# Kernel tuning notes

Hardware: AMD Instinct MI355X
Metric: run time of the kernel (lower is better)

The kernel has to match this reference:

```python
import jax, jax.numpy as jnp
import numpy as np

B, T, C = 2, 4096, 512
H = 8
D = C // H  # head_dim = 64


def setup_inputs() -> dict:
    key = jax.random.key(0)
    ks = jax.random.split(key, 9)
    s = 0.02
    return {
        "x": jax.random.normal(ks[0], (B, T, C), dtype=jnp.float32),
        "wq": jax.random.normal(ks[1], (C, C), dtype=jnp.float32) * s,
        "bq": jnp.zeros((C,), dtype=jnp.float32),
        "wk": jax.random.normal(ks[2], (C, C), dtype=jnp.float32) * s,
        "bk": jnp.zeros((C,), dtype=jnp.float32),
        "wv": jax.random.normal(ks[3], (C, C), dtype=jnp.float32) * s,
        "bv": jnp.zeros((C,), dtype=jnp.float32),
        "wo": jax.random.normal(ks[4], (C, C), dtype=jnp.float32) * s,
        "bo": jnp.zeros((C,), dtype=jnp.float32),
    }


def reference(x, wq, bq, wk, bk, wv, bv, wo, bo):
    Bx, Tx, Cx = x.shape
    # projections: y = x @ W^T + b (torch Linear convention: W is [out, in])
    q = (x @ wq.T + bq).reshape(Bx, Tx, H, D).transpose(0, 2, 1, 3)  # [B,H,T,D]
    k = (x @ wk.T + bk).reshape(Bx, Tx, H, D).transpose(0, 2, 1, 3)
    v = (x @ wv.T + bv).reshape(Bx, Tx, H, D).transpose(0, 2, 1, 3)
    scores = jnp.einsum("bhqd,bhkd->bhqk", q, k) * (D ** -0.5)  # [B,H,T,T]
    causal = jnp.tril(jnp.ones((Tx, Tx), dtype=bool))
    scores = jnp.where(causal, scores, -jnp.inf)
    weights = jax.nn.softmax(scores, axis=-1)
    o = jnp.einsum("bhqk,bhkd->bhqd", weights, v)  # [B,H,T,D]
    o = o.transpose(0, 2, 1, 3).reshape(Bx, Tx, Cx)
    return o @ wo.T + bo
```

## Files before the change

kernel.cpp:

```cpp
#include <hip/hip_runtime.h>
#include <math.h>

static constexpr int Bb = 2;
static constexpr int Tt = 4096;
static constexpr int Cc = 512;
static constexpr int Hh = 8;
static constexpr int Dd = 64;
static constexpr int Mtot = Bb * Tt;

#define QSCALE 0.1803368801111f
#define NTICK 1024

typedef __attribute__((ext_vector_type(8)))  short   short8;
typedef __attribute__((ext_vector_type(4)))  float   f32x4;
typedef __attribute__((ext_vector_type(16))) float   f32x16;
typedef __attribute__((ext_vector_type(4)))  unsigned int   uint4v;
typedef __attribute__((ext_vector_type(4)))  unsigned short ushort4v;

__device__ inline unsigned short f2bf(float f) {
    unsigned int u = __float_as_uint(f);
    u += 0x7fffu + ((u >> 16) & 1u);
    return (unsigned short)(u >> 16);
}
__device__ inline float bf2f(unsigned short u) {
    return __uint_as_float((unsigned int)u << 16);
}

__device__ inline unsigned int cvtpk_bf16(float a, float b) {
    unsigned int r;
    asm("v_cvt_pk_bf16_f32 %0, %1, %2" : "=v"(r) : "v"(a), "v"(b));
    return r;
}

__device__ inline int SW(int row) { return (row ^ (row >> 3)) & 7; }

__device__ inline void gload16(const void* g, void* lds) {
    __builtin_amdgcn_global_load_lds(
        (const __attribute__((address_space(1))) void*)g,
        (__attribute__((address_space(3))) void*)lds, 16, 0, 0);
}

__global__ __launch_bounds__(256)
void cast_f32_bf16(const float* __restrict__ src, unsigned short* __restrict__ dst,
                   int* __restrict__ ctr) {
    if (blockIdx.x == 0 && threadIdx.x == 0) *ctr = 0;
    const size_t i = ((size_t)blockIdx.x * 256 + threadIdx.x) * 8;
    const float4 a = *reinterpret_cast<const float4*>(src + i);
    const float4 b = *reinterpret_cast<const float4*>(src + i + 4);
    short8 o;
    o[0] = (short)f2bf(a.x); o[1] = (short)f2bf(a.y);
    o[2] = (short)f2bf(a.z); o[3] = (short)f2bf(a.w);
    o[4] = (short)f2bf(b.x); o[5] = (short)f2bf(b.y);
    o[6] = (short)f2bf(b.z); o[7] = (short)f2bf(b.w);
    *reinterpret_cast<short8*>(dst + i) = o;
}

__global__ __launch_bounds__(256)
void cast_w4(const float* __restrict__ w0, const float* __restrict__ w1,
             const float* __restrict__ w2, const float* __restrict__ w3,
             unsigned short* __restrict__ dst) {
    const float* srcs[4] = {w0, w1, w2, w3};
    const float* s = srcs[blockIdx.y];
    unsigned short* d = dst + (size_t)blockIdx.y * (Cc * Cc);
    const size_t i = ((size_t)blockIdx.x * 256 + threadIdx.x) * 8;
    const float4 a = *reinterpret_cast<const float4*>(s + i);
    const float4 b = *reinterpret_cast<const float4*>(s + i + 4);
    short8 o;
    o[0] = (short)f2bf(a.x); o[1] = (short)f2bf(a.y);
    o[2] = (short)f2bf(a.z); o[3] = (short)f2bf(a.w);
    o[4] = (short)f2bf(b.x); o[5] = (short)f2bf(b.y);
    o[6] = (short)f2bf(b.z); o[7] = (short)f2bf(b.w);
    *reinterpret_cast<short8*>(d + i) = o;
}

__global__ __launch_bounds__(256)
void proj_qkv(const unsigned short* __restrict__ A, const unsigned short* __restrict__ Wall,
              const float* __restrict__ bq, const float* __restrict__ bk,
              const float* __restrict__ bv,
              unsigned short* __restrict__ qo, unsigned short* __restrict__ ko,
              unsigned short* __restrict__ vo) {
    __shared__ unsigned short As[128][32];
    __shared__ unsigned short Bs[128][32];

    const int which = blockIdx.z;
    const unsigned short* Wb = Wall + (size_t)which * Cc * Cc;
    const float* bias = (which == 0) ? bq : (which == 1) ? bk : bv;
    unsigned short* outp = (which == 0) ? qo : (which == 1) ? ko : vo;
    const float scale = (which == 0) ? QSCALE : 1.0f;

    const int tid = threadIdx.x;
    const int lane = tid & 63;
    const int w = tid >> 6;
    const int wr = w >> 1, wc = w & 1;
    const int l15 = lane & 15, lg = lane >> 4;
    const int m0 = blockIdx.x * 128, n0 = blockIdx.y * 128;

    f32x4 acc[4][4] = {};

    for (int k0 = 0; k0 < Cc; k0 += 32) {
        #pragma unroll
        for (int i = 0; i < 2; ++i) {
            const int idx = tid + i * 256;
            const int row = idx >> 2, g = idx & 3;
            *reinterpret_cast<short8*>(&As[row][g * 8]) =
                *reinterpret_cast<const short8*>(&A[(size_t)(m0 + row) * Cc + k0 + g * 8]);
            *reinterpret_cast<short8*>(&Bs[row][g * 8]) =
                *reinterpret_cast<const short8*>(&Wb[(size_t)(n0 + row) * Cc + k0 + g * 8]);
        }
        __syncthreads();
        short8 a[4], b[4];
        #pragma unroll
        for (int mi = 0; mi < 4; ++mi)
            a[mi] = *reinterpret_cast<const short8*>(&As[wr * 64 + mi * 16 + l15][lg * 8]);
        #pragma unroll
        for (int nj = 0; nj < 4; ++nj)
            b[nj] = *reinterpret_cast<const short8*>(&Bs[wc * 64 + nj * 16 + l15][lg * 8]);
        #pragma unroll
        for (int mi = 0; mi < 4; ++mi)
            #pragma unroll
            for (int nj = 0; nj < 4; ++nj)
                acc[mi][nj] = __builtin_amdgcn_mfma_f32_16x16x32_bf16(a[mi], b[nj], acc[mi][nj], 0, 0, 0);
        __syncthreads();
    }

    #pragma unroll
    for (int mi = 0; mi < 4; ++mi) {
        #pragma unroll
        for (int nj = 0; nj < 4; ++nj) {
            const int col = n0 + wc * 64 + nj * 16 + l15;
            const float bvv = bias[col];
            if (which == 2) {
                const int mbase = m0 + wr * 64 + mi * 16 + lg * 4;
                const int b_ = mbase >> 12, t = mbase & (Tt - 1);
                const int h = col >> 6, d = col & 63;
                ushort4v o;
                #pragma unroll
                for (int r = 0; r < 4; ++r)
                    o[r] = f2bf(acc[mi][nj][r] + bvv);
                *reinterpret_cast<ushort4v*>(
                    &outp[(((size_t)b_ * Hh + h) * Dd + d) * Tt + t]) = o;
            } else {
                #pragma unroll
                for (int r = 0; r < 4; ++r) {
                    const int row = m0 + wr * 64 + mi * 16 + lg * 4 + r;
                    const int b_ = row >> 12, t = row & (Tt - 1);
                    const int h = col >> 6, d = col & 63;
                    outp[(((size_t)b_ * Hh + h) * Tt + t) * Dd + d] =
                        f2bf((acc[mi][nj][r] + bvv) * scale);
                }
            }
        }
    }
}

__global__ __launch_bounds__(256)
void proj_out(const unsigned short* __restrict__ A, const unsigned short* __restrict__ Wb,
              const float* __restrict__ bias, float* __restrict__ outp) {
    __shared__ unsigned short As[128][32];
    __shared__ unsigned short Bs[128][32];

    const int tid = threadIdx.x;
    const int lane = tid & 63;
    const int w = tid >> 6;
    const int wr = w >> 1, wc = w & 1;
    const int l15 = lane & 15, lg = lane >> 4;
    const int m0 = blockIdx.x * 128, n0 = blockIdx.y * 128;

    f32x4 acc[4][4] = {};

    for (int k0 = 0; k0 < Cc; k0 += 32) {
        #pragma unroll
        for (int i = 0; i < 2; ++i) {
            const int idx = tid + i * 256;
            const int row = idx >> 2, g = idx & 3;
            *reinterpret_cast<short8*>(&As[row][g * 8]) =
                *reinterpret_cast<const short8*>(&A[(size_t)(m0 + row) * Cc + k0 + g * 8]);
            *reinterpret_cast<short8*>(&Bs[row][g * 8]) =
                *reinterpret_cast<const short8*>(&Wb[(size_t)(n0 + row) * Cc + k0 + g * 8]);
        }
        __syncthreads();
        short8 a[4], b[4];
        #pragma unroll
        for (int mi = 0; mi < 4; ++mi)
            a[mi] = *reinterpret_cast<const short8*>(&As[wr * 64 + mi * 16 + l15][lg * 8]);
        #pragma unroll
        for (int nj = 0; nj < 4; ++nj)
            b[nj] = *reinterpret_cast<const short8*>(&Bs[wc * 64 + nj * 16 + l15][lg * 8]);
        #pragma unroll
        for (int mi = 0; mi < 4; ++mi)
            #pragma unroll
            for (int nj = 0; nj < 4; ++nj)
                acc[mi][nj] = __builtin_amdgcn_mfma_f32_16x16x32_bf16(a[mi], b[nj], acc[mi][nj], 0, 0, 0);
        __syncthreads();
    }

    #pragma unroll
    for (int mi = 0; mi < 4; ++mi) {
        #pragma unroll
        for (int nj = 0; nj < 4; ++nj) {
            const int col = n0 + wc * 64 + nj * 16 + l15;
            const float bv = bias[col];
            #pragma unroll
            for (int r = 0; r < 4; ++r) {
                const int row = m0 + wr * 64 + mi * 16 + lg * 4 + r;
                outp[(size_t)row * Cc + col] = acc[mi][nj][r] + bv;
            }
        }
    }
}

__global__ __launch_bounds__(512)
void attn_mfma(const unsigned short* __restrict__ qb, const unsigned short* __restrict__ kb,
               const unsigned short* __restrict__ vtb,
               unsigned short* __restrict__ opart, float* __restrict__ lp,
               int* __restrict__ ctr) {
    __shared__ unsigned short Ks[3][64][64];
    __shared__ unsigned short Vts[3][64][64];
    __shared__ int tkt;

    const int tid = threadIdx.x;
    const int w = tid >> 6;
    const int lane = tid & 63;
    const int l31 = lane & 31, hi = lane >> 5;

    const int r0 = (w << 3) + (lane >> 3);
    const int gk0 = ((lane & 7) ^ SW(r0)) * 8;

    for (;;) {
        __syncthreads();
        if (tid == 0) tkt = atomicAdd(ctr, 1);
        __syncthreads();
        const int t = tkt;
        if (t >= NTICK) break;

        const int qt = 15 - (t >> 6);
        const int ch = (t >> 4) & 3;
        const int bh = t & 15;
        const int t0 = (qt + 1) * ch;
        const int t1 = (qt + 1) * (ch + 1);

        const int qg = qt * 256 + w * 32 + l31;

        short8 qf[4];
        {
            const unsigned short* qp = qb + ((size_t)bh * Tt + qg) * Dd + hi * 8;
            #pragma unroll
            for (int sl = 0; sl < 4; ++sl)
                qf[sl] = *reinterpret_cast<const short8*>(qp + sl * 16);
        }

        const unsigned short* kb_h = kb + (size_t)bh * Tt * Dd;
        const unsigned short* vt_h = vtb + (size_t)bh * Dd * Tt;

        auto STAGE = [&](int kt_, int slot) {
            const int n64 = kt_ * 64;
            gload16(kb_h + (size_t)(n64 + r0) * Dd + gk0, &Ks[slot][(w << 3)][0]);
            gload16(vt_h + (size_t)r0 * Tt + n64 + gk0, &Vts[slot][(w << 3)][0]);
        };

        f32x16 oacc[2] = {};
        float lrow = 0.f;

        const int qmax_w = qt * 256 + w * 32 + 31;
        const int qmin_w = qt * 256 + w * 32;

        STAGE(t0, 0);
        if (t0 + 1 < t1) STAGE(t0 + 1, 1);

        int cur = 0;
        for (int kt = t0; kt < t1; ++kt) {
            if (kt + 1 < t1) {
                asm volatile("s_waitcnt vmcnt(2)" ::: "memory");
            } else {
                asm volatile("s_waitcnt vmcnt(0)" ::: "memory");
            }
            __builtin_amdgcn_s_barrier();
            __builtin_amdgcn_sched_barrier(0);

            if (kt + 2 < t1) {
                const int stg = (cur + 2 >= 3) ? (cur - 1) : (cur + 2);
                STAGE(kt + 2, stg);
            }

            if (kt * 64 <= qmax_w) {
                f32x16 sacc[2];
                __builtin_amdgcn_s_setprio(1);
                #pragma unroll
                for (int f = 0; f < 2; ++f) {
                    f32x16 z = {};
                    const int krow = f * 32 + l31;
                    const int sw = SW(krow);
                    #pragma unroll
                    for (int sl = 0; sl < 4; ++sl) {
                        const short8 kf = *reinterpret_cast<const short8*>(
                            &Ks[cur][krow][((2 * sl + hi) ^ sw) * 8]);
                        z = __builtin_amdgcn_mfma_f32_32x32x16_bf16(kf, qf[sl], z, 0, 0, 0);
                    }
                    sacc[f] = z;
                }
                __builtin_amdgcn_s_setprio(0);

                if (kt * 64 + 63 > qmin_w) {
                    #pragma unroll
                    for (int f = 0; f < 2; ++f)
                        #pragma unroll
                        for (int r = 0; r < 16; ++r) {
                            const int kvg = kt * 64 + f * 32 + (r & 3) + 8 * (r >> 2) + 4 * hi;
                            if (kvg > qg) sacc[f][r] = -INFINITY;
                        }
                }

                #pragma unroll
                for (int f = 0; f < 2; ++f)
                    #pragma unroll
                    for (int r = 0; r < 16; ++r)
                        sacc[f][r] = exp2f(sacc[f][r]);

                float t16[16];
                #pragma unroll
                for (int r = 0; r < 16; ++r) t16[r] = sacc[0][r] + sacc[1][r];
                #pragma unroll
                for (int r = 0; r < 8; ++r) t16[r] += t16[r + 8];
                #pragma unroll
                for (int r = 0; r < 4; ++r) t16[r] += t16[r + 4];
                t16[0] += t16[2];
                t16[1] += t16[3];
                lrow += t16[0] + t16[1];

                #pragma unroll
                for (int f = 0; f < 2; ++f) {
                    #pragma unroll
                    for (int s2 = 0; s2 < 2; ++s2) {
                        const int b0 = s2 * 8;
                        unsigned int c01 = cvtpk_bf16(sacc[f][b0 + 0], sacc[f][b0 + 1]);
                        unsigned int c23 = cvtpk_bf16(sacc[f][b0 + 2], sacc[f][b0 + 3]);
                        unsigned int c45 = cvtpk_bf16(sacc[f][b0 + 4], sacc[f][b0 + 5]);
                        unsigned int c67 = cvtpk_bf16(sacc[f][b0 + 6], sacc[f][b0 + 7]);
                        asm("v_permlane32_swap_b32 %0, %1" : "+v"(c01), "+v"(c45));
                        asm("v_permlane32_swap_b32 %0, %1" : "+v"(c23), "+v"(c67));
                        uint4v paw;
                        paw[0] = c01; paw[1] = c23; paw[2] = c45; paw[3] = c67;
                        const short8 pa = *reinterpret_cast<short8*>(&paw);
                        const int g = 4 * f + 2 * s2;
                        __builtin_amdgcn_s_setprio(1);
                        #pragma unroll
                        for (int nb = 0; nb < 2; ++nb) {
                            const int vrow = nb * 32 + l31;
                            const short8 vf = *reinterpret_cast<const short8*>(
                                &Vts[cur][vrow][((g + hi) ^ SW(vrow)) * 8]);
                            oacc[nb] = __builtin_amdgcn_mfma_f32_32x32x16_bf16(pa, vf, oacc[nb], 0, 0, 0);
                        }
                        __builtin_amdgcn_s_setprio(0);
                    }
                }
            }

            cur = (cur == 2) ? 0 : cur + 1;
        }

        const float lf = lrow + __shfl_xor(lrow, 32);
        const size_t pbase = ((size_t)ch * 16 + bh) * Tt;
        if (hi == 0) lp[pbase + qg] = lf;
        #pragma unroll
        for (int r = 0; r < 16; ++r) {
            const int qr = (r & 3) + 8 * (r >> 2) + 4 * hi;
            const int tg = qt * 256 + w * 32 + qr;
            unsigned short* dst = opart + (pbase + tg) * 64 + l31;
            dst[0]  = f2bf(oacc[0][r]);
            dst[32] = f2bf(oacc[1][r]);
        }
    }
}

__global__ __launch_bounds__(256)
void combine(const unsigned short* __restrict__ opart, const float* __restrict__ lp,
             unsigned short* __restrict__ ob) {
    const int tid = threadIdx.x;
    const int row = (int)blockIdx.x * 16 + (tid >> 4);
    const int c4 = (tid & 15) * 4;
    const size_t cs = (size_t)16 * Tt;

    const float inv = 1.f / (lp[row] + lp[cs + row] + lp[2 * cs + row] + lp[3 * cs + row]);

    const ushort4v p0 = *reinterpret_cast<const ushort4v*>(&opart[(0 * cs + row) * 64 + c4]);
    const ushort4v p1 = *reinterpret_cast<const ushort4v*>(&opart[(1 * cs + row) * 64 + c4]);
    const ushort4v p2 = *reinterpret_cast<const ushort4v*>(&opart[(2 * cs + row) * 64 + c4]);
    const ushort4v p3 = *reinterpret_cast<const ushort4v*>(&opart[(3 * cs + row) * 64 + c4]);

    ushort4v o;
    #pragma unroll
    for (int e = 0; e < 4; ++e)
        o[e] = f2bf((bf2f(p0[e]) + bf2f(p1[e]) + bf2f(p2[e]) + bf2f(p3[e])) * inv);

    const int bh = row >> 12, t = row & (Tt - 1);
    const int b_ = bh >> 3, h = bh & 7;
    *reinterpret_cast<ushort4v*>(&ob[((size_t)b_ * Tt + t) * Cc + h * Dd + c4]) = o;
}

extern "C" void kernel_launch(void* const* d_in, const int* in_sizes, int n_in,
                              void* d_out, int out_size, void* d_ws, size_t ws_size,
                              hipStream_t stream) {
    const float* x  = (const float*)d_in[0];
    const float* wq = (const float*)d_in[1];
    const float* bq = (const float*)d_in[2];
    const float* wk = (const float*)d_in[3];
    const float* bk = (const float*)d_in[4];
    const float* wv = (const float*)d_in[5];
    const float* bv = (const float*)d_in[6];
    const float* wo = (const float*)d_in[7];
    const float* bo = (const float*)d_in[8];
    float* out = (float*)d_out;

    const size_t nTok = (size_t)Mtot * Cc;
    const size_t nW   = (size_t)Cc * Cc;

    unsigned short* xb    = (unsigned short*)d_ws;
    unsigned short* wqb   = xb + nTok;
    unsigned short* wob   = wqb + 3 * nW;
    unsigned short* qbuf  = wqb + 4 * nW;
    unsigned short* kbuf  = qbuf + nTok;
    unsigned short* vtbuf = kbuf + nTok;
    unsigned short* oattb = vtbuf + nTok;
    unsigned short* opart = oattb + nTok;
    float* lp  = (float*)(opart + (size_t)4 * 16 * Tt * 64);
    int*   ctr = (int*)(lp + (size_t)4 * 16 * Tt);

    cast_f32_bf16<<<dim3((unsigned)(nTok / 8 / 256)), 256, 0, stream>>>(x, xb, ctr);
    cast_w4<<<dim3((unsigned)(nW / 8 / 256), 4), 256, 0, stream>>>(wq, wk, wv, wo, wqb);

    proj_qkv<<<dim3(Mtot / 128, Cc / 128, 3), 256, 0, stream>>>(
        xb, wqb, bq, bk, bv, qbuf, kbuf, vtbuf);

    attn_mfma<<<dim3(512), 512, 0, stream>>>(qbuf, kbuf, vtbuf, opart, lp, ctr);

    combine<<<dim3(16 * Tt / 16), 256, 0, stream>>>(opart, lp, oattb);

    proj_out<<<dim3(Mtot / 128, Cc / 128), 256, 0, stream>>>(oattb, wob, bo, out);
}
```

Baseline: 148.5 us.

## Merge cast kernels, fuse combine into out-proj, retile attention to 128-row tiles

Several changes land together. The two cast kernels become one launch. The partial-output combine (sum over chunks, divide by row sum) moves into proj_out's A-tile load, which removes a kernel and the oattb round trip through memory. Projections now load B tiles (and A tiles in proj_qkv) with direct global-to-LDS loads using an XOR swizzle. Attention goes from 256-row query tiles with 8 waves and triple buffering to 128-row tiles with 4 waves, double buffering and twice as many tickets, with the KV range split unevenly into four chunks. Risks are redundant combine loads per N-block in proj_out and less latency hiding from the shallower pipeline.

New measurement: 156.3 us. +5.2%, slower.

```diff
diff --git a/kernel.cpp b/kernel.cpp
--- a/kernel.cpp
+++ b/kernel.cpp
@@ -9,7 +9,7 @@
 static constexpr int Mtot = Bb * Tt;
 
 #define QSCALE 0.1803368801111f
-#define NTICK 1024
+#define NTICK 2048
 
 typedef __attribute__((ext_vector_type(8)))  short   short8;
 typedef __attribute__((ext_vector_type(4)))  float   f32x4;
@@ -41,10 +41,26 @@
 }
 
 __global__ __launch_bounds__(256)
-void cast_f32_bf16(const float* __restrict__ src, unsigned short* __restrict__ dst,
-                   int* __restrict__ ctr) {
-    if (blockIdx.x == 0 && threadIdx.x == 0) *ctr = 0;
-    const size_t i = ((size_t)blockIdx.x * 256 + threadIdx.x) * 8;
+void cast_all(const float* __restrict__ x,
+              const float* __restrict__ w0, const float* __restrict__ w1,
+              const float* __restrict__ w2, const float* __restrict__ w3,
+              unsigned short* __restrict__ xb, unsigned short* __restrict__ wb,
+              int* __restrict__ ctr) {
+    const int bid = (int)blockIdx.x;
+    if (bid == 0 && threadIdx.x == 0) *ctr = 0;
+    const float* src;
+    unsigned short* dst;
+    size_t i;
+    if (bid < 2048) {
+        src = x; dst = xb;
+        i = ((size_t)bid * 256 + threadIdx.x) * 8;
+    } else {
+        const float* srcs[4] = {w0, w1, w2, w3};
+        const int wi = (bid - 2048) >> 7;
+        src = srcs[wi];
+        dst = wb + (size_t)wi * (Cc * Cc);
+        i = ((size_t)((bid - 2048) & 127) * 256 + threadIdx.x) * 8;
+    }
     const float4 a = *reinterpret_cast<const float4*>(src + i);
     const float4 b = *reinterpret_cast<const float4*>(src + i + 4);
     short8 o;
@@ -56,24 +72,6 @@
 }
 
 __global__ __launch_bounds__(256)
-void cast_w4(const float* __restrict__ w0, const float* __restrict__ w1,
-             const float* __restrict__ w2, const float* __restrict__ w3,
-             unsigned short* __restrict__ dst) {
-    const float* srcs[4] = {w0, w1, w2, w3};
-    const float* s = srcs[blockIdx.y];
-    unsigned short* d = dst + (size_t)blockIdx.y * (Cc * Cc);
-    const size_t i = ((size_t)blockIdx.x * 256 + threadIdx.x) * 8;
-    const float4 a = *reinterpret_cast<const float4*>(s + i);
-    const float4 b = *reinterpret_cast<const float4*>(s + i + 4);
-    short8 o;
-    o[0] = (short)f2bf(a.x); o[1] = (short)f2bf(a.y);
-    o[2] = (short)f2bf(a.z); o[3] = (short)f2bf(a.w);
-    o[4] = (short)f2bf(b.x); o[5] = (short)f2bf(b.y);
-    o[6] = (short)f2bf(b.z); o[7] = (short)f2bf(b.w);
-    *reinterpret_cast<short8*>(d + i) = o;
-}
-
-__global__ __launch_bounds__(256)
 void proj_qkv(const unsigned short* __restrict__ A, const unsigned short* __restrict__ Wall,
               const float* __restrict__ bq, const float* __restrict__ bk,
               const float* __restrict__ bv,
@@ -95,26 +93,28 @@
     const int l15 = lane & 15, lg = lane >> 4;
     const int m0 = blockIdx.x * 128, n0 = blockIdx.y * 128;
 
+    const int srow = (w << 4) + (lane >> 2);
+    const int sg   = (lane & 3);
+
     f32x4 acc[4][4] = {};
 
     for (int k0 = 0; k0 < Cc; k0 += 32) {
         #pragma unroll
         for (int i = 0; i < 2; ++i) {
-            const int idx = tid + i * 256;
-            const int row = idx >> 2, g = idx & 3;
-            *reinterpret_cast<short8*>(&As[row][g * 8]) =
-                *reinterpret_cast<const short8*>(&A[(size_t)(m0 + row) * Cc + k0 + g * 8]);
-            *reinterpret_cast<short8*>(&Bs[row][g * 8]) =
-                *reinterpret_cast<const short8*>(&Wb[(size_t)(n0 + row) * Cc + k0 + g * 8]);
+            const int row = 64 * i + srow;
+            const int gc = ((sg ^ (row & 3))) * 8;
+            gload16(&A[(size_t)(m0 + row) * Cc + k0 + gc], &As[64 * i + (w << 4)][0]);
+            gload16(&Wb[(size_t)(n0 + row) * Cc + k0 + gc], &Bs[64 * i + (w << 4)][0]);
         }
         __syncthreads();
         short8 a[4], b[4];
+        const int rg = (lg ^ (l15 & 3)) * 8;
         #pragma unroll
         for (int mi = 0; mi < 4; ++mi)
-            a[mi] = *reinterpret_cast<const short8*>(&As[wr * 64 + mi * 16 + l15][lg * 8]);
+            a[mi] = *reinterpret_cast<const short8*>(&As[wr * 64 + mi * 16 + l15][rg]);
         #pragma unroll
         for (int nj = 0; nj < 4; ++nj)
-            b[nj] = *reinterpret_cast<const short8*>(&Bs[wc * 64 + nj * 16 + l15][lg * 8]);
+            b[nj] = *reinterpret_cast<const short8*>(&Bs[wc * 64 + nj * 16 + l15][rg]);
         #pragma unroll
         for (int mi = 0; mi < 4; ++mi)
             #pragma unroll
@@ -154,7 +154,8 @@
 }
 
 __global__ __launch_bounds__(256)
-void proj_out(const unsigned short* __restrict__ A, const unsigned short* __restrict__ Wb,
+void proj_out(const unsigned short* __restrict__ opart, const float* __restrict__ lp,
+              const unsigned short* __restrict__ Wb,
               const float* __restrict__ bias, float* __restrict__ outp) {
     __shared__ unsigned short As[128][32];
     __shared__ unsigned short Bs[128][32];
@@ -166,26 +167,63 @@
     const int l15 = lane & 15, lg = lane >> 4;
     const int m0 = blockIdx.x * 128, n0 = blockIdx.y * 128;
 
+    const int row_a = tid >> 1;
+    const int cc0 = (tid & 1) * 16;
+    const int m = m0 + row_a;
+    const int b_a = m >> 12, t_a = m & (Tt - 1);
+    const size_t cs = (size_t)16 * Tt;
+
+    const int srow = (w << 4) + (lane >> 2);
+    const int sg   = (lane & 3);
+
     f32x4 acc[4][4] = {};
 
     for (int k0 = 0; k0 < Cc; k0 += 32) {
+        {
+            const int c0 = k0 + cc0;
+            const int h = c0 >> 6, d0 = c0 & 63;
+            const int bhp = b_a * Hh + h;
+            const size_t rbase = (size_t)bhp * Tt + t_a;
+            const float lsum = lp[rbase] + lp[cs + rbase] +
+                               lp[2 * cs + rbase] + lp[3 * cs + rbase];
+            const float inv = 1.f / lsum;
+            float s[16] = {};
+            #pragma unroll
+            for (int ch = 0; ch < 4; ++ch) {
+                const unsigned short* p = &opart[(ch * cs + rbase) * 64 + d0];
+                const short8 lo = *reinterpret_cast<const short8*>(p);
+                const short8 hi8 = *reinterpret_cast<const short8*>(p + 8);
+                #pragma unroll
+                for (int e = 0; e < 8; ++e) {
+                    s[e]     += bf2f((unsigned short)lo[e]);
+                    s[e + 8] += bf2f((unsigned short)hi8[e]);
+                }
+            }
+            short8 o0, o1;
+            #pragma unroll
+            for (int e = 0; e < 8; ++e) {
+                o0[e] = (short)f2bf(s[e] * inv);
+                o1[e] = (short)f2bf(s[e + 8] * inv);
+            }
+            const int g0 = (tid & 1) * 2;
+            *reinterpret_cast<short8*>(&As[row_a][((g0 ^ (row_a & 3))) * 8]) = o0;
+            *reinterpret_cast<short8*>(&As[row_a][(((g0 + 1) ^ (row_a & 3))) * 8]) = o1;
+        }
         #pragma unroll
         for (int i = 0; i < 2; ++i) {
-            const int idx = tid + i * 256;
-            const int row = idx >> 2, g = idx & 3;
-            *reinterpret_cast<short8*>(&As[row][g * 8]) =
-                *reinterpret_cast<const short8*>(&A[(size_t)(m0 + row) * Cc + k0 + g * 8]);
-            *reinterpret_cast<short8*>(&Bs[row][g * 8]) =
-                *reinterpret_cast<const short8*>(&Wb[(size_t)(n0 + row) * Cc + k0 + g * 8]);
+            const int row = 64 * i + srow;
+            const int gc = ((sg ^ (row & 3))) * 8;
+            gload16(&Wb[(size_t)(n0 + row) * Cc + k0 + gc], &Bs[64 * i + (w << 4)][0]);
         }
         __syncthreads();
         short8 a[4], b[4];
+        const int rg = (lg ^ (l15 & 3)) * 8;
         #pragma unroll
         for (int mi = 0; mi < 4; ++mi)
-            a[mi] = *reinterpret_cast<const short8*>(&As[wr * 64 + mi * 16 + l15][lg * 8]);
+            a[mi] = *reinterpret_cast<const short8*>(&As[wr * 64 + mi * 16 + l15][rg]);
         #pragma unroll
         for (int nj = 0; nj < 4; ++nj)
-            b[nj] = *reinterpret_cast<const short8*>(&Bs[wc * 64 + nj * 16 + l15][lg * 8]);
+            b[nj] = *reinterpret_cast<const short8*>(&Bs[wc * 64 + nj * 16 + l15][rg]);
         #pragma unroll
         for (int mi = 0; mi < 4; ++mi)
             #pragma unroll
@@ -209,13 +247,13 @@
     }
 }
 
-__global__ __launch_bounds__(512)
+__global__ __launch_bounds__(256)
 void attn_mfma(const unsigned short* __restrict__ qb, const unsigned short* __restrict__ kb,
                const unsigned short* __restrict__ vtb,
                unsigned short* __restrict__ opart, float* __restrict__ lp,
                int* __restrict__ ctr) {
-    __shared__ unsigned short Ks[3][64][64];
-    __shared__ unsigned short Vts[3][64][64];
+    __shared__ unsigned short Ks[2][64][64];
+    __shared__ unsigned short Vts[2][64][64];
     __shared__ int tkt;
 
     const int tid = threadIdx.x;
@@ -223,8 +261,10 @@
     const int lane = tid & 63;
     const int l31 = lane & 31, hi = lane >> 5;
 
-    const int r0 = (w << 3) + (lane >> 3);
+    const int r0 = (w << 4) + (lane >> 3);
+    const int r1 = r0 + 8;
     const int gk0 = ((lane & 7) ^ SW(r0)) * 8;
+    const int gk1 = ((lane & 7) ^ SW(r1)) * 8;
 
     for (;;) {
         __syncthreads();
@@ -233,129 +273,125 @@
         const int t = tkt;
         if (t >= NTICK) break;
 
-        const int qt = 15 - (t >> 6);
+        const int qt = 31 - (t >> 6);
         const int ch = (t >> 4) & 3;
         const int bh = t & 15;
-        const int t0 = (qt + 1) * ch;
-        const int t1 = (qt + 1) * (ch + 1);
-
-        const int qg = qt * 256 + w * 32 + l31;
-
-        short8 qf[4];
-        {
-            const unsigned short* qp = qb + ((size_t)bh * Tt + qg) * Dd + hi * 8;
-            #pragma unroll
-            for (int sl = 0; sl < 4; ++sl)
-                qf[sl] = *reinterpret_cast<const short8*>(qp + sl * 16);
-        }
-
-        const unsigned short* kb_h = kb + (size_t)bh * Tt * Dd;
-        const unsigned short* vt_h = vtb + (size_t)bh * Dd * Tt;
-
-        auto STAGE = [&](int kt_, int slot) {
-            const int n64 = kt_ * 64;
-            gload16(kb_h + (size_t)(n64 + r0) * Dd + gk0, &Ks[slot][(w << 3)][0]);
-            gload16(vt_h + (size_t)r0 * Tt + n64 + gk0, &Vts[slot][(w << 3)][0]);
-        };
+        const int n  = 2 * qt + 2;
+        const int t0 = (n * ch) >> 2;
+        const int t1 = (n * (ch + 1)) >> 2;
+
+        const int qg = qt * 128 + w * 32 + l31;
 
         f32x16 oacc[2] = {};
         float lrow = 0.f;
 
-        const int qmax_w = qt * 256 + w * 32 + 31;
-        const int qmin_w = qt * 256 + w * 32;
-
-        STAGE(t0, 0);
-        if (t0 + 1 < t1) STAGE(t0 + 1, 1);
-
-        int cur = 0;
-        for (int kt = t0; kt < t1; ++kt) {
-            if (kt + 1 < t1) {
-                asm volatile("s_waitcnt vmcnt(2)" ::: "memory");
-            } else {
+        if (t0 < t1) {
+            short8 qf[4];
+            {
+                const unsigned short* qp = qb + ((size_t)bh * Tt + qg) * Dd + hi * 8;
+                #pragma unroll
+                for (int sl = 0; sl < 4; ++sl)
+                    qf[sl] = *reinterpret_cast<const short8*>(qp + sl * 16);
+            }
+
+            const unsigned short* kb_h = kb + (size_t)bh * Tt * Dd;
+            const unsigned short* vt_h = vtb + (size_t)bh * Dd * Tt;
+
+            auto STAGE = [&](int kt_) {
+                const int n64 = kt_ * 64;
+                const int bufi = kt_ & 1;
+                gload16(kb_h + (size_t)(n64 + r0) * Dd + gk0, &Ks[bufi][(w << 4)][0]);
+                gload16(kb_h + (size_t)(n64 + r1) * Dd + gk1, &Ks[bufi][(w << 4) + 8][0]);
+                gload16(vt_h + (size_t)r0 * Tt + n64 + gk0, &Vts[bufi][(w << 4)][0]);
+                gload16(vt_h + (size_t)r1 * Tt + n64 + gk1, &Vts[bufi][(w << 4) + 8][0]);
+            };
+
+            const int qmax_w = qt * 128 + w * 32 + 31;
+            const int qmin_w = qt * 128 + w * 32;
+
+            STAGE(t0);
+
+            for (int kt = t0; kt < t1; ++kt) {
+                const int cur = kt & 1;
                 asm volatile("s_waitcnt vmcnt(0)" ::: "memory");
-            }
-            __builtin_amdgcn_s_barrier();
-            __builtin_amdgcn_sched_barrier(0);
-
-            if (kt + 2 < t1) {
-                const int stg = (cur + 2 >= 3) ? (cur - 1) : (cur + 2);
-                STAGE(kt + 2, stg);
-            }
-
-            if (kt * 64 <= qmax_w) {
-                f32x16 sacc[2];
-                __builtin_amdgcn_s_setprio(1);
-                #pragma unroll
-                for (int f = 0; f < 2; ++f) {
-                    f32x16 z = {};
-                    const int krow = f * 32 + l31;
-                    const int sw = SW(krow);
-                    #pragma unroll
-                    for (int sl = 0; sl < 4; ++sl) {
-                        const short8 kf = *reinterpret_cast<const short8*>(
-                            &Ks[cur][krow][((2 * sl + hi) ^ sw) * 8]);
-                        z = __builtin_amdgcn_mfma_f32_32x32x16_bf16(kf, qf[sl], z, 0, 0, 0);
+                __builtin_amdgcn_s_barrier();
+                __builtin_amdgcn_sched_barrier(0);
+
+                if (kt + 1 < t1) STAGE(kt + 1);
+
+                if (kt * 64 <= qmax_w) {
+                    f32x16 sacc[2];
+                    __builtin_amdgcn_s_setprio(1);
+                    #pragma unroll
+                    for (int f = 0; f < 2; ++f) {
+                        f32x16 z = {};
+                        const int krow = f * 32 + l31;
+                        const int sw = SW(krow);
+                        #pragma unroll
+                        for (int sl = 0; sl < 4; ++sl) {
+                            const short8 kf = *reinterpret_cast<const short8*>(
+                                &Ks[cur][krow][((2 * sl + hi) ^ sw) * 8]);
+                            z = __builtin_amdgcn_mfma_f32_32x32x16_bf16(kf, qf[sl], z, 0, 0, 0);
+                        }
+                        sacc[f] = z;
                     }
-                    sacc[f] = z;
-                }
-                __builtin_amdgcn_s_setprio(0);
-
-                if (kt * 64 + 63 > qmin_w) {
+                    __builtin_amdgcn_s_setprio(0);
+
+                    if (kt * 64 + 63 > qmin_w) {
+                        #pragma unroll
+                        for (int f = 0; f < 2; ++f)
+                            #pragma unroll
+                            for (int r = 0; r < 16; ++r) {
+                                const int kvg = kt * 64 + f * 32 + (r & 3) + 8 * (r >> 2) + 4 * hi;
+                                if (kvg > qg) sacc[f][r] = -INFINITY;
+                            }
+                    }
+
                     #pragma unroll
                     for (int f = 0; f < 2; ++f)
                         #pragma unroll
-                        for (int r = 0; r < 16; ++r) {
-                            const int kvg = kt * 64 + f * 32 + (r & 3) + 8 * (r >> 2) + 4 * hi;
-                            if (kvg > qg) sacc[f][r] = -INFINITY;
+                        for (int r = 0; r < 16; ++r)
+                            sacc[f][r] = exp2f(sacc[f][r]);
+
+                    float t16[16];
+                    #pragma unroll
+                    for (int r = 0; r < 16; ++r) t16[r] = sacc[0][r] + sacc[1][r];
+                    #pragma unroll
+                    for (int r = 0; r < 8; ++r) t16[r] += t16[r + 8];
+                    #pragma unroll
+                    for (int r = 0; r < 4; ++r) t16[r] += t16[r + 4];
+                    t16[0] += t16[2];
+                    t16[1] += t16[3];
+                    lrow += t16[0] + t16[1];
+
+                    #pragma unroll
+                    for (int f = 0; f < 2; ++f) {
+                        #pragma unroll
+                        for (int s2 = 0; s2 < 2; ++s2) {
+                            const int b0 = s2 * 8;
+                            unsigned int c01 = cvtpk_bf16(sacc[f][b0 + 0], sacc[f][b0 + 1]);
+                            unsigned int c23 = cvtpk_bf16(sacc[f][b0 + 2], sacc[f][b0 + 3]);
+                            unsigned int c45 = cvtpk_bf16(sacc[f][b0 + 4], sacc[f][b0 + 5]);
+                            unsigned int c67 = cvtpk_bf16(sacc[f][b0 + 6], sacc[f][b0 + 7]);
+                            asm("v_permlane32_swap_b32 %0, %1" : "+v"(c01), "+v"(c45));
+                            asm("v_permlane32_swap_b32 %0, %1" : "+v"(c23), "+v"(c67));
+                            uint4v paw;
+                            paw[0] = c01; paw[1] = c23; paw[2] = c45; paw[3] = c67;
+                            const short8 pa = *reinterpret_cast<short8*>(&paw);
+                            const int g = 4 * f + 2 * s2;
+                            __builtin_amdgcn_s_setprio(1);
+                            #pragma unroll
+                            for (int nb = 0; nb < 2; ++nb) {
+                                const int vrow = nb * 32 + l31;
+                                const short8 vf = *reinterpret_cast<const short8*>(
+                                    &Vts[cur][vrow][((g + hi) ^ SW(vrow)) * 8]);
+                                oacc[nb] = __builtin_amdgcn_mfma_f32_32x32x16_bf16(pa, vf, oacc[nb], 0, 0, 0);
+                            }
+                            __builtin_amdgcn_s_setprio(0);
                         }
-                }
-
-                #pragma unroll
-                for (int f = 0; f < 2; ++f)
-                    #pragma unroll
-                    for (int r = 0; r < 16; ++r)
-                        sacc[f][r] = exp2f(sacc[f][r]);
-
-                float t16[16];
-                #pragma unroll
-                for (int r = 0; r < 16; ++r) t16[r] = sacc[0][r] + sacc[1][r];
-                #pragma unroll
-                for (int r = 0; r < 8; ++r) t16[r] += t16[r + 8];
-                #pragma unroll
-                for (int r = 0; r < 4; ++r) t16[r] += t16[r + 4];
-                t16[0] += t16[2];
-                t16[1] += t16[3];
-                lrow += t16[0] + t16[1];
-
-                #pragma unroll
-                for (int f = 0; f < 2; ++f) {
-                    #pragma unroll
-                    for (int s2 = 0; s2 < 2; ++s2) {
-                        const int b0 = s2 * 8;
-                        unsigned int c01 = cvtpk_bf16(sacc[f][b0 + 0], sacc[f][b0 + 1]);
-                        unsigned int c23 = cvtpk_bf16(sacc[f][b0 + 2], sacc[f][b0 + 3]);
-                        unsigned int c45 = cvtpk_bf16(sacc[f][b0 + 4], sacc[f][b0 + 5]);
-                        unsigned int c67 = cvtpk_bf16(sacc[f][b0 + 6], sacc[f][b0 + 7]);
-                        asm("v_permlane32_swap_b32 %0, %1" : "+v"(c01), "+v"(c45));
-                        asm("v_permlane32_swap_b32 %0, %1" : "+v"(c23), "+v"(c67));
-                        uint4v paw;
-                        paw[0] = c01; paw[1] = c23; paw[2] = c45; paw[3] = c67;
-                        const short8 pa = *reinterpret_cast<short8*>(&paw);
-                        const int g = 4 * f + 2 * s2;
-                        __builtin_amdgcn_s_setprio(1);
-                        #pragma unroll
-                        for (int nb = 0; nb < 2; ++nb) {
-                            const int vrow = nb * 32 + l31;
-                            const short8 vf = *reinterpret_cast<const short8*>(
-                                &Vts[cur][vrow][((g + hi) ^ SW(vrow)) * 8]);
-                            oacc[nb] = __builtin_amdgcn_mfma_f32_32x32x16_bf16(pa, vf, oacc[nb], 0, 0, 0);
-                        }
-                        __builtin_amdgcn_s_setprio(0);
                     }
                 }
             }
-
-            cur = (cur == 2) ? 0 : cur + 1;
         }
 
         const float lf = lrow + __shfl_xor(lrow, 32);
@@ -364,37 +400,12 @@
         #pragma unroll
         for (int r = 0; r < 16; ++r) {
             const int qr = (r & 3) + 8 * (r >> 2) + 4 * hi;
-            const int tg = qt * 256 + w * 32 + qr;
+            const int tg = qt * 128 + w * 32 + qr;
             unsigned short* dst = opart + (pbase + tg) * 64 + l31;
             dst[0]  = f2bf(oacc[0][r]);
             dst[32] = f2bf(oacc[1][r]);
         }
     }
-}
-
-__global__ __launch_bounds__(256)
-void combine(const unsigned short* __restrict__ opart, const float* __restrict__ lp,
-             unsigned short* __restrict__ ob) {
-    const int tid = threadIdx.x;
-    const int row = (int)blockIdx.x * 16 + (tid >> 4);
-    const int c4 = (tid & 15) * 4;
-    const size_t cs = (size_t)16 * Tt;
-
-    const float inv = 1.f / (lp[row] + lp[cs + row] + lp[2 * cs + row] + lp[3 * cs + row]);
-
-    const ushort4v p0 = *reinterpret_cast<const ushort4v*>(&opart[(0 * cs + row) * 64 + c4]);
-    const ushort4v p1 = *reinterpret_cast<const ushort4v*>(&opart[(1 * cs + row) * 64 + c4]);
-    const ushort4v p2 = *reinterpret_cast<const ushort4v*>(&opart[(2 * cs + row) * 64 + c4]);
-    const ushort4v p3 = *reinterpret_cast<const ushort4v*>(&opart[(3 * cs + row) * 64 + c4]);
-
-    ushort4v o;
-    #pragma unroll
-    for (int e = 0; e < 4; ++e)
-        o[e] = f2bf((bf2f(p0[e]) + bf2f(p1[e]) + bf2f(p2[e]) + bf2f(p3[e])) * inv);
-
-    const int bh = row >> 12, t = row & (Tt - 1);
-    const int b_ = bh >> 3, h = bh & 7;
-    *reinterpret_cast<ushort4v*>(&ob[((size_t)b_ * Tt + t) * Cc + h * Dd + c4]) = o;
 }
 
 extern "C" void kernel_launch(void* const* d_in, const int* in_sizes, int n_in,
@@ -420,20 +431,16 @@
     unsigned short* qbuf  = wqb + 4 * nW;
     unsigned short* kbuf  = qbuf + nTok;
     unsigned short* vtbuf = kbuf + nTok;
-    unsigned short* oattb = vtbuf + nTok;
-    unsigned short* opart = oattb + nTok;
+    unsigned short* opart = vtbuf + nTok;
     float* lp  = (float*)(opart + (size_t)4 * 16 * Tt * 64);
     int*   ctr = (int*)(lp + (size_t)4 * 16 * Tt);
 
-    cast_f32_bf16<<<dim3((unsigned)(nTok / 8 / 256)), 256, 0, stream>>>(x, xb, ctr);
-    cast_w4<<<dim3((unsigned)(nW / 8 / 256), 4), 256, 0, stream>>>(wq, wk, wv, wo, wqb);
+    cast_all<<<dim3(2560), 256, 0, stream>>>(x, wq, wk, wv, wo, xb, wqb, ctr);
 
     proj_qkv<<<dim3(Mtot / 128, Cc / 128, 3), 256, 0, stream>>>(
         xb, wqb, bq, bk, bv, qbuf, kbuf, vtbuf);
 
-    attn_mfma<<<dim3(512), 512, 0, stream>>>(qbuf, kbuf, vtbuf, opart, lp, ctr);
-
-    combine<<<dim3(16 * Tt / 16), 256, 0, stream>>>(opart, lp, oattb);
-
-    proj_out<<<dim3(Mtot / 128, Cc / 128), 256, 0, stream>>>(oattb, wob, bo, out);
-}
+    attn_mfma<<<dim3(1024), 256, 0, stream>>>(qbuf, kbuf, vtbuf, opart, lp, ctr);
+
+    proj_out<<<dim3(Mtot / 128, Cc / 128), 256, 0, stream>>>(opart, lp, wob, bo, out);
+}
```
